# Kernel tuning notes

Hardware: AMD Instinct MI355X
Metric: run time of the kernel (lower is better)

Reference implementation:

```python
import jax, jax.numpy as jnp
import numpy as np

N_NODES = 65536
N_EDGES = 1048576
IN_CH, HID_CH, OUT_CH = 300, 64, 20
DROPOUT_P = 0.5


def setup_inputs() -> dict:
    key = jax.random.key(0)
    ks = jax.random.split(key, 6)
    x = jax.random.normal(ks[0], (N_NODES, IN_CH), dtype=jnp.float32)
    edge_index = jax.random.randint(ks[1], (2, N_EDGES), 0, N_NODES, dtype=jnp.int64)
    edge_weight = jax.random.uniform(ks[2], (N_EDGES,), dtype=jnp.float32)
    # Glorot-ish init for linear weights (PyG lin has no bias; GCNConv adds its own bias)
    W1 = jax.random.normal(ks[3], (IN_CH, HID_CH), dtype=jnp.float32) / np.sqrt(IN_CH)
    b1 = jnp.zeros((HID_CH,), dtype=jnp.float32)
    W2 = jax.random.normal(ks[4], (HID_CH, OUT_CH), dtype=jnp.float32) / np.sqrt(HID_CH)
    b2 = jnp.zeros((OUT_CH,), dtype=jnp.float32)
    return {"x": x, "edge_index": edge_index, "edge_weight": edge_weight,
            "W1": W1, "b1": b1, "W2": W2, "b2": b2}


def _gcn_conv(x, src, dst, edge_weight, W, b, num_nodes):
    # GCNConv with add_self_loops=False, normalize=False:
    #   h = x @ W; out[i] = sum_{e: dst(e)=i} w_e * h[src(e)]; out += b
    h = x @ W                                   # [N, C_out]
    msg = h[src] * edge_weight[:, None]         # [E, C_out]
    agg = jax.ops.segment_sum(msg, dst, num_segments=num_nodes)
    return agg + b


def reference(x, edge_index, edge_weight, W1, b1, W2, b2):
    num_nodes = x.shape[0]
    src, dst = edge_index[0], edge_index[1]
    h = _gcn_conv(x, src, dst, edge_weight, W1, b1, num_nodes)
    h = jax.nn.relu(h)
    # dropout p=0.5, training=True, deterministic fixed key
    keep = jax.random.bernoulli(jax.random.key(42), 1.0 - DROPOUT_P, h.shape)
    h = jnp.where(keep, h / (1.0 - DROPOUT_P), 0.0)
    out = _gcn_conv(h, src, dst, edge_weight, W2, b2, num_nodes)
    return out
```

## Files before the change

kernel.cpp:

```cpp
#include <hip/hip_runtime.h>

#define N_NODES 65536
#define N_EDGES 1048576
#define NB 256
#define CAP 4608
#define EPB_A 4096
#define BLK_A (N_EDGES / EPB_A)
#define EPT_A (EPB_A / 256)

typedef __attribute__((ext_vector_type(8))) short short8v;
typedef __attribute__((ext_vector_type(4))) float float4v;

__device__ __forceinline__ unsigned short f2bf(float f) {
  unsigned u = __float_as_uint(f);
  unsigned r = u + 0x7FFFu + ((u >> 16) & 1u);
  return (unsigned short)(r >> 16);
}
__device__ __forceinline__ float bflo(unsigned u) { return __uint_as_float(u << 16); }
__device__ __forceinline__ float bfhi(unsigned u) { return __uint_as_float(u & 0xFFFF0000u); }

__device__ __forceinline__ bool keep_mask(unsigned idx) {
  const unsigned k0 = 0u, k1 = 42u;
  const unsigned k2 = 0x1BD11BDAu ^ k0 ^ k1;
  unsigned x0 = 0u;
  unsigned x1 = idx;
  x0 += k0; x1 += k1;
#define TF_ROUND(r) { x0 += x1; x1 = (x1 << (r)) | (x1 >> (32 - (r))); x1 ^= x0; }
  TF_ROUND(13) TF_ROUND(15) TF_ROUND(26) TF_ROUND(6)
  x0 += k1; x1 += k2 + 1u;
  TF_ROUND(17) TF_ROUND(29) TF_ROUND(16) TF_ROUND(24)
  x0 += k2; x1 += k0 + 2u;
  TF_ROUND(13) TF_ROUND(15) TF_ROUND(26) TF_ROUND(6)
  x0 += k0; x1 += k1 + 3u;
  TF_ROUND(17) TF_ROUND(29) TF_ROUND(16) TF_ROUND(24)
  x0 += k1; x1 += k2 + 4u;
  TF_ROUND(13) TF_ROUND(15) TF_ROUND(26) TF_ROUND(6)
  x0 += k2; x1 += k0 + 5u;
#undef TF_ROUND
  return ((x0 ^ x1) & 0x80000000u) == 0u;
}

__global__ __launch_bounds__(256) void prep_w1(const float* __restrict__ W1,
                                               unsigned short* __restrict__ Wt,
                                               unsigned* __restrict__ gcur) {
  if (blockIdx.x == 0) gcur[threadIdx.x] = 0u;
  int i = blockIdx.x * 256 + threadIdx.x;
  if (i >= 64 * 320) return;
  int ch = i / 320, k = i % 320;
  float v = (k < 300) ? W1[k * 64 + ch] : 0.0f;
  Wt[i] = f2bf(v);
}

__global__ __launch_bounds__(256) void bin_pass(const int* __restrict__ ei,
                                                const float* __restrict__ ew,
                                                unsigned* __restrict__ gcur,
                                                uint2* __restrict__ binned) {
  __shared__ unsigned cnt[NB], lofs[NB], lcur[NB], gbase[NB];
  __shared__ uint2 stage[EPB_A];
  const int t = threadIdx.x;
  const int e0 = blockIdx.x * EPB_A;
  cnt[t] = 0u;
  lcur[t] = 0u;
  __syncthreads();
  unsigned pk[EPT_A], pw[EPT_A];
#pragma unroll
  for (int j = 0; j < EPT_A; ++j) {
    int e = e0 + t + j * 256;
    unsigned s = (unsigned)ei[e];
    unsigned d = (unsigned)ei[N_EDGES + e];
    pk[j] = s | (d << 16);
    pw[j] = __float_as_uint(ew[e]);
    atomicAdd(&cnt[d >> 8], 1u);
  }
  __syncthreads();
  lofs[t] = cnt[t];
  __syncthreads();
  for (int d = 1; d < NB; d <<= 1) {
    unsigned u = (t >= d) ? lofs[t - d] : 0u;
    __syncthreads();
    lofs[t] += u;
    __syncthreads();
  }
  unsigned incl = lofs[t];
  lofs[t] = incl - cnt[t];
  gbase[t] = (unsigned)t * CAP + atomicAdd(&gcur[t], cnt[t]);
  __syncthreads();
#pragma unroll
  for (int j = 0; j < EPT_A; ++j) {
    unsigned b = pk[j] >> 24;
    unsigned slot = lofs[b] + atomicAdd(&lcur[b], 1u);
    stage[slot] = make_uint2(pk[j], pw[j]);
  }
  __syncthreads();
  for (int s = t; s < EPB_A; s += 256) {
    uint2 u = stage[s];
    unsigned b = u.x >> 24;
    binned[gbase[b] + ((unsigned)s - lofs[b])] = u;
  }
}

__global__ __launch_bounds__(256) void bucket_sort(const unsigned* __restrict__ gcur,
                                                   const uint2* __restrict__ binned,
                                                   unsigned* __restrict__ sortedc,
                                                   unsigned* __restrict__ offs_p) {
  __shared__ uint2 eLDS[CAP];
  __shared__ unsigned cnt[NB], cur[NB];
  const int t = threadIdx.x;
  const int b = blockIdx.x;
  const unsigned lo = (unsigned)b * CAP;
  const unsigned n_edges = gcur[b];
  cnt[t] = 0u;
  __syncthreads();
  for (unsigned i = t; i < n_edges; i += 256) {
    uint2 u = binned[lo + i];
    eLDS[i] = u;
    atomicAdd(&cnt[(u.x >> 16) & 255u], 1u);
  }
  __syncthreads();
  cur[t] = cnt[t];
  __syncthreads();
  for (int d = 1; d < NB; d <<= 1) {
    unsigned u = (t >= d) ? cur[t - d] : 0u;
    __syncthreads();
    cur[t] += u;
    __syncthreads();
  }
  unsigned excl = cur[t] - cnt[t];
  offs_p[b * NB + t] = (lo + excl) | (cnt[t] << 21);
  __syncthreads();
  cur[t] = excl;
  __syncthreads();
  for (unsigned i = t; i < n_edges; i += 256) {
    uint2 u = eLDS[i];
    unsigned lo8 = (u.x >> 16) & 255u;
    unsigned p = lo + atomicAdd(&cur[lo8], 1u);
    sortedc[p] = (u.x & 0xFFFFu) | ((unsigned)f2bf(__uint_as_float(u.y)) << 16);
  }
}

__global__ __launch_bounds__(256) void gemm1_mfma(const float* __restrict__ x,
                                                  const unsigned short* __restrict__ Wt,
                                                  unsigned short* __restrict__ h1b) {
  __shared__ unsigned short As[64][72];
  __shared__ unsigned short Bs[64][72];
  const int t = threadIdx.x;
  const int node0 = blockIdx.x * 64;
  const int wave = t >> 6, lane = t & 63;
  const int quad = lane >> 4, l16 = lane & 15;
  float4v acc[4] = {{0.f,0.f,0.f,0.f},{0.f,0.f,0.f,0.f},{0.f,0.f,0.f,0.f},{0.f,0.f,0.f,0.f}};

  for (int kt = 0; kt < 5; ++kt) {
    const int k0 = kt * 64;
    for (int f = t; f < 1024; f += 256) {
      int node = f >> 4;
      int k = (f & 15) * 4;
      uint2 packed;
      if (k0 + k < 300) {
        float4 v = *(const float4*)(x + (size_t)(node0 + node) * 300 + k0 + k);
        packed.x = (unsigned)f2bf(v.x) | ((unsigned)f2bf(v.y) << 16);
        packed.y = (unsigned)f2bf(v.z) | ((unsigned)f2bf(v.w) << 16);
      } else {
        packed.x = 0u; packed.y = 0u;
      }
      *(uint2*)&As[node][k] = packed;
    }
    for (int f = t; f < 512; f += 256) {
      int ch = f >> 3;
      int kq = f & 7;
      uint4 v = *(const uint4*)(Wt + (size_t)ch * 320 + k0 + kq * 8);
      *(uint4*)&Bs[ch][kq * 8] = v;
    }
    __syncthreads();
    short8v a0 = *(const short8v*)&As[wave * 16 + l16][quad * 8];
    short8v a1 = *(const short8v*)&As[wave * 16 + l16][32 + quad * 8];
#pragma unroll
    for (int nt = 0; nt < 4; ++nt) {
      short8v b0 = *(const short8v*)&Bs[nt * 16 + l16][quad * 8];
      short8v b1 = *(const short8v*)&Bs[nt * 16 + l16][32 + quad * 8];
      acc[nt] = __builtin_amdgcn_mfma_f32_16x16x32_bf16(a0, b0, acc[nt], 0, 0, 0);
      acc[nt] = __builtin_amdgcn_mfma_f32_16x16x32_bf16(a1, b1, acc[nt], 0, 0, 0);
    }
    __syncthreads();
  }
#pragma unroll
  for (int nt = 0; nt < 4; ++nt) {
#pragma unroll
    for (int r = 0; r < 4; ++r) {
      h1b[(size_t)(node0 + wave * 16 + quad * 4 + r) * 64 + nt * 16 + l16] = f2bf(acc[nt][r]);
    }
  }
}

__global__ __launch_bounds__(256) void agg1_gemm2(const unsigned* __restrict__ offs_p,
                                                  const unsigned* __restrict__ sortedc,
                                                  const unsigned short* __restrict__ h1b,
                                                  const float* __restrict__ b1,
                                                  const float* __restrict__ W2,
                                                  unsigned* __restrict__ g32u) {
  __shared__ float h2[16][68];
  __shared__ float w2t[20][68];
  const int t = threadIdx.x;
  const int node0 = blockIdx.x * 16;
  for (int i = t; i < 64 * 20; i += 256) {
    w2t[i % 20][i / 20] = W2[i];
  }
  const int n = t >> 4, cg = t & 15;
  const int node = node0 + n;
  const unsigned op = offs_p[node];
  const unsigned s = op & 0x1FFFFFu;
  const unsigned e_end = s + (op >> 21);
  float4 acc = *(const float4*)(b1 + cg * 4);
  unsigned i = s;
  for (; i + 8 <= e_end; i += 8) {
    unsigned e0 = sortedc[i],     e1 = sortedc[i + 1], e2 = sortedc[i + 2], e3 = sortedc[i + 3];
    unsigned e4 = sortedc[i + 4], e5 = sortedc[i + 5], e6 = sortedc[i + 6], e7 = sortedc[i + 7];
    uint2 v0 = *(const uint2*)(h1b + ((size_t)(e0 & 0xFFFFu)) * 64 + cg * 4);
    uint2 v1 = *(const uint2*)(h1b + ((size_t)(e1 & 0xFFFFu)) * 64 + cg * 4);
    uint2 v2 = *(const uint2*)(h1b + ((size_t)(e2 & 0xFFFFu)) * 64 + cg * 4);
    uint2 v3 = *(const uint2*)(h1b + ((size_t)(e3 & 0xFFFFu)) * 64 + cg * 4);
    uint2 v4 = *(const uint2*)(h1b + ((size_t)(e4 & 0xFFFFu)) * 64 + cg * 4);
    uint2 v5 = *(const uint2*)(h1b + ((size_t)(e5 & 0xFFFFu)) * 64 + cg * 4);
    uint2 v6 = *(const uint2*)(h1b + ((size_t)(e6 & 0xFFFFu)) * 64 + cg * 4);
    uint2 v7 = *(const uint2*)(h1b + ((size_t)(e7 & 0xFFFFu)) * 64 + cg * 4);
    float w0 = bfhi(e0), w1 = bfhi(e1), w2 = bfhi(e2), w3 = bfhi(e3);
    float w4 = bfhi(e4), w5 = bfhi(e5), w6 = bfhi(e6), w7 = bfhi(e7);
    acc.x = fmaf(w0, bflo(v0.x), acc.x); acc.y = fmaf(w0, bfhi(v0.x), acc.y);
    acc.z = fmaf(w0, bflo(v0.y), acc.z); acc.w = fmaf(w0, bfhi(v0.y), acc.w);
    acc.x = fmaf(w1, bflo(v1.x), acc.x); acc.y = fmaf(w1, bfhi(v1.x), acc.y);
    acc.z = fmaf(w1, bflo(v1.y), acc.z); acc.w = fmaf(w1, bfhi(v1.y), acc.w);
    acc.x = fmaf(w2, bflo(v2.x), acc.x); acc.y = fmaf(w2, bfhi(v2.x), acc.y);
    acc.z = fmaf(w2, bflo(v2.y), acc.z); acc.w = fmaf(w2, bfhi(v2.y), acc.w);
    acc.x = fmaf(w3, bflo(v3.x), acc.x); acc.y = fmaf(w3, bfhi(v3.x), acc.y);
    acc.z = fmaf(w3, bflo(v3.y), acc.z); acc.w = fmaf(w3, bfhi(v3.y), acc.w);
    acc.x = fmaf(w4, bflo(v4.x), acc.x); acc.y = fmaf(w4, bfhi(v4.x), acc.y);
    acc.z = fmaf(w4, bflo(v4.y), acc.z); acc.w = fmaf(w4, bfhi(v4.y), acc.w);
    acc.x = fmaf(w5, bflo(v5.x), acc.x); acc.y = fmaf(w5, bfhi(v5.x), acc.y);
    acc.z = fmaf(w5, bflo(v5.y), acc.z); acc.w = fmaf(w5, bfhi(v5.y), acc.w);
    acc.x = fmaf(w6, bflo(v6.x), acc.x); acc.y = fmaf(w6, bfhi(v6.x), acc.y);
    acc.z = fmaf(w6, bflo(v6.y), acc.z); acc.w = fmaf(w6, bfhi(v6.y), acc.w);
    acc.x = fmaf(w7, bflo(v7.x), acc.x); acc.y = fmaf(w7, bfhi(v7.x), acc.y);
    acc.z = fmaf(w7, bflo(v7.y), acc.z); acc.w = fmaf(w7, bfhi(v7.y), acc.w);
  }
  for (; i < e_end; ++i) {
    unsigned e0 = sortedc[i];
    uint2 v0 = *(const uint2*)(h1b + ((size_t)(e0 & 0xFFFFu)) * 64 + cg * 4);
    float w0 = bfhi(e0);
    acc.x = fmaf(w0, bflo(v0.x), acc.x); acc.y = fmaf(w0, bfhi(v0.x), acc.y);
    acc.z = fmaf(w0, bflo(v0.y), acc.z); acc.w = fmaf(w0, bfhi(v0.y), acc.w);
  }
  const unsigned gi = (unsigned)node * 64u + (unsigned)cg * 4u;
  float r[4] = {acc.x, acc.y, acc.z, acc.w};
#pragma unroll
  for (int j = 0; j < 4; ++j) {
    float v = fmaxf(r[j], 0.0f);
    h2[n][cg * 4 + j] = keep_mask(gi + j) ? v * 2.0f : 0.0f;
  }
  __syncthreads();
  float d0 = 0.0f, d1 = 0.0f;
  if (cg < 10) {
    const int c0 = cg * 2, c1 = cg * 2 + 1;
#pragma unroll
    for (int k = 0; k < 64; k += 4) {
      float4 hv = *(const float4*)(&h2[n][k]);
      float4 w0 = *(const float4*)(&w2t[c0][k]);
      float4 w1 = *(const float4*)(&w2t[c1][k]);
      d0 = fmaf(hv.x, w0.x, d0); d0 = fmaf(hv.y, w0.y, d0);
      d0 = fmaf(hv.z, w0.z, d0); d0 = fmaf(hv.w, w0.w, d0);
      d1 = fmaf(hv.x, w1.x, d1); d1 = fmaf(hv.y, w1.y, d1);
      d1 = fmaf(hv.z, w1.z, d1); d1 = fmaf(hv.w, w1.w, d1);
    }
  }
  unsigned packed = (cg < 10) ? ((unsigned)f2bf(d0) | ((unsigned)f2bf(d1) << 16)) : 0u;
  g32u[(size_t)node * 16 + cg] = packed;
}

__global__ __launch_bounds__(256) void aggregate2(const unsigned* __restrict__ offs_p,
                                                  const unsigned* __restrict__ sortedc,
                                                  const unsigned* __restrict__ g32u,
                                                  const float* __restrict__ b2,
                                                  float* __restrict__ out) {
  const int t = threadIdx.x;
  const int n = blockIdx.x * 16 + (t >> 4);
  const int cg = t & 15;
  const unsigned op = offs_p[n];
  const unsigned s = op & 0x1FFFFFu;
  const unsigned e_end = s + (op >> 21);
  float ax = 0.0f, ay = 0.0f;
  unsigned i = s;
  for (; i + 8 <= e_end; i += 8) {
    unsigned e0 = sortedc[i],     e1 = sortedc[i + 1], e2 = sortedc[i + 2], e3 = sortedc[i + 3];
    unsigned e4 = sortedc[i + 4], e5 = sortedc[i + 5], e6 = sortedc[i + 6], e7 = sortedc[i + 7];
    unsigned v0 = g32u[(size_t)(e0 & 0xFFFFu) * 16 + cg];
    unsigned v1 = g32u[(size_t)(e1 & 0xFFFFu) * 16 + cg];
    unsigned v2 = g32u[(size_t)(e2 & 0xFFFFu) * 16 + cg];
    unsigned v3 = g32u[(size_t)(e3 & 0xFFFFu) * 16 + cg];
    unsigned v4 = g32u[(size_t)(e4 & 0xFFFFu) * 16 + cg];
    unsigned v5 = g32u[(size_t)(e5 & 0xFFFFu) * 16 + cg];
    unsigned v6 = g32u[(size_t)(e6 & 0xFFFFu) * 16 + cg];
    unsigned v7 = g32u[(size_t)(e7 & 0xFFFFu) * 16 + cg];
    float w0 = bfhi(e0), w1 = bfhi(e1), w2 = bfhi(e2), w3 = bfhi(e3);
    float w4 = bfhi(e4), w5 = bfhi(e5), w6 = bfhi(e6), w7 = bfhi(e7);
    ax = fmaf(w0, bflo(v0), ax); ay = fmaf(w0, bfhi(v0), ay);
    ax = fmaf(w1, bflo(v1), ax); ay = fmaf(w1, bfhi(v1), ay);
    ax = fmaf(w2, bflo(v2), ax); ay = fmaf(w2, bfhi(v2), ay);
    ax = fmaf(w3, bflo(v3), ax); ay = fmaf(w3, bfhi(v3), ay);
    ax = fmaf(w4, bflo(v4), ax); ay = fmaf(w4, bfhi(v4), ay);
    ax = fmaf(w5, bflo(v5), ax); ay = fmaf(w5, bfhi(v5), ay);
    ax = fmaf(w6, bflo(v6), ax); ay = fmaf(w6, bfhi(v6), ay);
    ax = fmaf(w7, bflo(v7), ax); ay = fmaf(w7, bfhi(v7), ay);
  }
  for (; i < e_end; ++i) {
    unsigned e0 = sortedc[i];
    unsigned v0 = g32u[(size_t)(e0 & 0xFFFFu) * 16 + cg];
    float w0 = bfhi(e0);
    ax = fmaf(w0, bflo(v0), ax); ay = fmaf(w0, bfhi(v0), ay);
  }
  if (cg < 10) {
    float2 o = make_float2(ax + b2[cg * 2], ay + b2[cg * 2 + 1]);
    *(float2*)(out + (size_t)n * 20 + cg * 2) = o;
  }
}

extern "C" void kernel_launch(void* const* d_in, const int* in_sizes, int n_in,
                              void* d_out, int out_size, void* d_ws, size_t ws_size,
                              hipStream_t stream) {
  const float* x  = (const float*)d_in[0];
  const int*   ei = (const int*)d_in[1];
  const float* ew = (const float*)d_in[2];
  const float* W1 = (const float*)d_in[3];
  const float* b1 = (const float*)d_in[4];
  const float* W2 = (const float*)d_in[5];
  const float* b2 = (const float*)d_in[6];
  float* out = (float*)d_out;

  unsigned short* h1b     = (unsigned short*)d_ws;
  unsigned*       g32u    = (unsigned*)(h1b + (size_t)N_NODES * 64);
  uint2*          binned  = (uint2*)(g32u + (size_t)N_NODES * 16);
  unsigned*       sortedc = (unsigned*)(binned + (size_t)NB * CAP);
  unsigned*       offs_p  = sortedc + (size_t)NB * CAP;
  unsigned short* Wt      = (unsigned short*)(offs_p + N_NODES);
  unsigned*       gcur    = (unsigned*)(Wt + 64 * 320);

  prep_w1<<<(64 * 320 + 255) / 256, 256, 0, stream>>>(W1, Wt, gcur);
  bin_pass<<<BLK_A, 256, 0, stream>>>(ei, ew, gcur, binned);
  bucket_sort<<<NB, 256, 0, stream>>>(gcur, binned, sortedc, offs_p);
  gemm1_mfma<<<N_NODES / 64, 256, 0, stream>>>(x, Wt, h1b);
  agg1_gemm2<<<N_NODES / 16, 256, 0, stream>>>(offs_p, sortedc, h1b, b1, W2, g32u);
  aggregate2<<<N_NODES / 16, 256, 0, stream>>>(offs_p, sortedc, g32u, b2, out);
}
```

Before: 223.2 us.

## Co-schedule GEMM1 halves with binning and bucket-sort kernels

The independent GEMM1 node-tile work is split in two halves and merged into the binning and bucket-sort launches, with extra blocks selected by block index. This lets the compute-heavy GEMM overlap the atomic- and memory-bound edge sorting, and it removes one kernel launch. The fused kernels use the larger shared-memory size of the two branches for every block, which can lower occupancy for the GEMM blocks.

After: 224.1 us. About the same (+0.4%).

```diff
diff --git a/kernel.cpp b/kernel.cpp
--- a/kernel.cpp
+++ b/kernel.cpp
@@ -7,6 +7,7 @@
 #define EPB_A 4096
 #define BLK_A (N_EDGES / EPB_A)
 #define EPT_A (EPB_A / 256)
+#define GHALF 512
 
 typedef __attribute__((ext_vector_type(8))) short short8v;
 typedef __attribute__((ext_vector_type(4))) float float4v;
@@ -51,14 +52,18 @@
   Wt[i] = f2bf(v);
 }
 
-__global__ __launch_bounds__(256) void bin_pass(const int* __restrict__ ei,
-                                                const float* __restrict__ ew,
-                                                unsigned* __restrict__ gcur,
-                                                uint2* __restrict__ binned) {
-  __shared__ unsigned cnt[NB], lofs[NB], lcur[NB], gbase[NB];
-  __shared__ uint2 stage[EPB_A];
-  const int t = threadIdx.x;
-  const int e0 = blockIdx.x * EPB_A;
+__device__ __forceinline__ void bin_body(unsigned char* smraw, int bid,
+                                         const int* __restrict__ ei,
+                                         const float* __restrict__ ew,
+                                         unsigned* __restrict__ gcur,
+                                         uint2* __restrict__ binned) {
+  uint2*    stage = (uint2*)smraw;
+  unsigned* cnt   = (unsigned*)(smraw + 32768);
+  unsigned* lofs  = cnt + NB;
+  unsigned* lcur  = lofs + NB;
+  unsigned* gbase = lcur + NB;
+  const int t = threadIdx.x;
+  const int e0 = bid * EPB_A;
   cnt[t] = 0u;
   lcur[t] = 0u;
   __syncthreads();
@@ -99,14 +104,15 @@
   }
 }
 
-__global__ __launch_bounds__(256) void bucket_sort(const unsigned* __restrict__ gcur,
-                                                   const uint2* __restrict__ binned,
-                                                   unsigned* __restrict__ sortedc,
-                                                   unsigned* __restrict__ offs_p) {
-  __shared__ uint2 eLDS[CAP];
-  __shared__ unsigned cnt[NB], cur[NB];
-  const int t = threadIdx.x;
-  const int b = blockIdx.x;
+__device__ __forceinline__ void bucket_body(unsigned char* smraw, int b,
+                                            const unsigned* __restrict__ gcur,
+                                            const uint2* __restrict__ binned,
+                                            unsigned* __restrict__ sortedc,
+                                            unsigned* __restrict__ offs_p) {
+  uint2*    eLDS = (uint2*)smraw;
+  unsigned* cnt  = (unsigned*)(smraw + 36864);
+  unsigned* cur  = cnt + NB;
+  const int t = threadIdx.x;
   const unsigned lo = (unsigned)b * CAP;
   const unsigned n_edges = gcur[b];
   cnt[t] = 0u;
@@ -138,13 +144,14 @@
   }
 }
 
-__global__ __launch_bounds__(256) void gemm1_mfma(const float* __restrict__ x,
-                                                  const unsigned short* __restrict__ Wt,
-                                                  unsigned short* __restrict__ h1b) {
-  __shared__ unsigned short As[64][72];
-  __shared__ unsigned short Bs[64][72];
-  const int t = threadIdx.x;
-  const int node0 = blockIdx.x * 64;
+__device__ __forceinline__ void gemm1_body(unsigned char* smraw, int nb,
+                                           const float* __restrict__ x,
+                                           const unsigned short* __restrict__ Wt,
+                                           unsigned short* __restrict__ h1b) {
+  unsigned short (*As)[72] = (unsigned short (*)[72])smraw;
+  unsigned short (*Bs)[72] = (unsigned short (*)[72])(smraw + 9216);
+  const int t = threadIdx.x;
+  const int node0 = nb * 64;
   const int wave = t >> 6, lane = t & 63;
   const int quad = lane >> 4, l16 = lane & 15;
   float4v acc[4] = {{0.f,0.f,0.f,0.f},{0.f,0.f,0.f,0.f},{0.f,0.f,0.f,0.f},{0.f,0.f,0.f,0.f}};
@@ -188,6 +195,36 @@
     for (int r = 0; r < 4; ++r) {
       h1b[(size_t)(node0 + wave * 16 + quad * 4 + r) * 64 + nt * 16 + l16] = f2bf(acc[nt][r]);
     }
+  }
+}
+
+__global__ __launch_bounds__(256) void fusedA(const int* __restrict__ ei,
+                                              const float* __restrict__ ew,
+                                              unsigned* __restrict__ gcur,
+                                              uint2* __restrict__ binned,
+                                              const float* __restrict__ x,
+                                              const unsigned short* __restrict__ Wt,
+                                              unsigned short* __restrict__ h1b) {
+  __shared__ __align__(16) unsigned char sm[36864];
+  if (blockIdx.x < BLK_A) {
+    bin_body(sm, blockIdx.x, ei, ew, gcur, binned);
+  } else {
+    gemm1_body(sm, blockIdx.x - BLK_A, x, Wt, h1b);
+  }
+}
+
+__global__ __launch_bounds__(256) void fusedB(const unsigned* __restrict__ gcur,
+                                              const uint2* __restrict__ binned,
+                                              unsigned* __restrict__ sortedc,
+                                              unsigned* __restrict__ offs_p,
+                                              const float* __restrict__ x,
+                                              const unsigned short* __restrict__ Wt,
+                                              unsigned short* __restrict__ h1b) {
+  __shared__ __align__(16) unsigned char sm[38912];
+  if (blockIdx.x < NB) {
+    bucket_body(sm, blockIdx.x, gcur, binned, sortedc, offs_p);
+  } else {
+    gemm1_body(sm, GHALF + (blockIdx.x - NB), x, Wt, h1b);
   }
 }
 
@@ -342,9 +379,8 @@
   unsigned*       gcur    = (unsigned*)(Wt + 64 * 320);
 
   prep_w1<<<(64 * 320 + 255) / 256, 256, 0, stream>>>(W1, Wt, gcur);
-  bin_pass<<<BLK_A, 256, 0, stream>>>(ei, ew, gcur, binned);
-  bucket_sort<<<NB, 256, 0, stream>>>(gcur, binned, sortedc, offs_p);
-  gemm1_mfma<<<N_NODES / 64, 256, 0, stream>>>(x, Wt, h1b);
+  fusedA<<<BLK_A + GHALF, 256, 0, stream>>>(ei, ew, gcur, binned, x, Wt, h1b);
+  fusedB<<<NB + GHALF, 256, 0, stream>>>(gcur, binned, sortedc, offs_p, x, Wt, h1b);
   agg1_gemm2<<<N_NODES / 16, 256, 0, stream>>>(offs_p, sortedc, h1b, b1, W2, g32u);
   aggregate2<<<N_NODES / 16, 256, 0, stream>>>(offs_p, sortedc, g32u, b2, out);
 }
```

## Replace two-pass bucket sort with atomic slot scatter fused with GEMM1

Applied to the files above, without the earlier changes.

The bin_pass and bucket_sort kernels are replaced by one pass. Each edge takes a per-destination slot with a global atomic counter and is written straight into a fixed 64-slot row per node. That scatter runs in the same launch as the GEMM1 MFMA blocks, so the two independent stages can overlap, and prep now also zeroes the counters. This drops a kernel, the intermediate binned buffer and the LDS prefix scans. In exchange, edges beyond 64 per node are silently dropped, within-node edge order becomes nondeterministic, and the edge list is spread over a larger, sparser buffer.

Result: slower. 236.2 us (+5.8%).

```diff
diff --git a/kernel.cpp b/kernel.cpp
--- a/kernel.cpp
+++ b/kernel.cpp
@@ -2,11 +2,11 @@
 
 #define N_NODES 65536
 #define N_EDGES 1048576
-#define NB 256
-#define CAP 4608
-#define EPB_A 4096
-#define BLK_A (N_EDGES / EPB_A)
-#define EPT_A (EPB_A / 256)
+#define SLOTS 64
+#define SCAT_BLK 512
+#define SCAT_EPB (N_EDGES / SCAT_BLK)
+#define SCAT_EPT (SCAT_EPB / 256)
+#define GEMM_BLK (N_NODES / 64)
 
 typedef __attribute__((ext_vector_type(8))) short short8v;
 typedef __attribute__((ext_vector_type(4))) float float4v;
@@ -40,111 +40,29 @@
   return ((x0 ^ x1) & 0x80000000u) == 0u;
 }
 
-__global__ __launch_bounds__(256) void prep_w1(const float* __restrict__ W1,
-                                               unsigned short* __restrict__ Wt,
-                                               unsigned* __restrict__ gcur) {
-  if (blockIdx.x == 0) gcur[threadIdx.x] = 0u;
-  int i = blockIdx.x * 256 + threadIdx.x;
+__global__ __launch_bounds__(256) void prep(const float* __restrict__ W1,
+                                            unsigned short* __restrict__ Wt,
+                                            unsigned* __restrict__ cnt) {
+  const int b = blockIdx.x;
+  if (b < 256) {
+    cnt[b * 256 + threadIdx.x] = 0u;
+    return;
+  }
+  int i = (b - 256) * 256 + threadIdx.x;
   if (i >= 64 * 320) return;
   int ch = i / 320, k = i % 320;
   float v = (k < 300) ? W1[k * 64 + ch] : 0.0f;
   Wt[i] = f2bf(v);
 }
 
-__global__ __launch_bounds__(256) void bin_pass(const int* __restrict__ ei,
-                                                const float* __restrict__ ew,
-                                                unsigned* __restrict__ gcur,
-                                                uint2* __restrict__ binned) {
-  __shared__ unsigned cnt[NB], lofs[NB], lcur[NB], gbase[NB];
-  __shared__ uint2 stage[EPB_A];
+__device__ __forceinline__ void gemm1_body(unsigned char* smraw, int nb,
+                                           const float* __restrict__ x,
+                                           const unsigned short* __restrict__ Wt,
+                                           unsigned short* __restrict__ h1b) {
+  unsigned short (*As)[72] = (unsigned short (*)[72])smraw;
+  unsigned short (*Bs)[72] = (unsigned short (*)[72])(smraw + 9216);
   const int t = threadIdx.x;
-  const int e0 = blockIdx.x * EPB_A;
-  cnt[t] = 0u;
-  lcur[t] = 0u;
-  __syncthreads();
-  unsigned pk[EPT_A], pw[EPT_A];
-#pragma unroll
-  for (int j = 0; j < EPT_A; ++j) {
-    int e = e0 + t + j * 256;
-    unsigned s = (unsigned)ei[e];
-    unsigned d = (unsigned)ei[N_EDGES + e];
-    pk[j] = s | (d << 16);
-    pw[j] = __float_as_uint(ew[e]);
-    atomicAdd(&cnt[d >> 8], 1u);
-  }
-  __syncthreads();
-  lofs[t] = cnt[t];
-  __syncthreads();
-  for (int d = 1; d < NB; d <<= 1) {
-    unsigned u = (t >= d) ? lofs[t - d] : 0u;
-    __syncthreads();
-    lofs[t] += u;
-    __syncthreads();
-  }
-  unsigned incl = lofs[t];
-  lofs[t] = incl - cnt[t];
-  gbase[t] = (unsigned)t * CAP + atomicAdd(&gcur[t], cnt[t]);
-  __syncthreads();
-#pragma unroll
-  for (int j = 0; j < EPT_A; ++j) {
-    unsigned b = pk[j] >> 24;
-    unsigned slot = lofs[b] + atomicAdd(&lcur[b], 1u);
-    stage[slot] = make_uint2(pk[j], pw[j]);
-  }
-  __syncthreads();
-  for (int s = t; s < EPB_A; s += 256) {
-    uint2 u = stage[s];
-    unsigned b = u.x >> 24;
-    binned[gbase[b] + ((unsigned)s - lofs[b])] = u;
-  }
-}
-
-__global__ __launch_bounds__(256) void bucket_sort(const unsigned* __restrict__ gcur,
-                                                   const uint2* __restrict__ binned,
-                                                   unsigned* __restrict__ sortedc,
-                                                   unsigned* __restrict__ offs_p) {
-  __shared__ uint2 eLDS[CAP];
-  __shared__ unsigned cnt[NB], cur[NB];
-  const int t = threadIdx.x;
-  const int b = blockIdx.x;
-  const unsigned lo = (unsigned)b * CAP;
-  const unsigned n_edges = gcur[b];
-  cnt[t] = 0u;
-  __syncthreads();
-  for (unsigned i = t; i < n_edges; i += 256) {
-    uint2 u = binned[lo + i];
-    eLDS[i] = u;
-    atomicAdd(&cnt[(u.x >> 16) & 255u], 1u);
-  }
-  __syncthreads();
-  cur[t] = cnt[t];
-  __syncthreads();
-  for (int d = 1; d < NB; d <<= 1) {
-    unsigned u = (t >= d) ? cur[t - d] : 0u;
-    __syncthreads();
-    cur[t] += u;
-    __syncthreads();
-  }
-  unsigned excl = cur[t] - cnt[t];
-  offs_p[b * NB + t] = (lo + excl) | (cnt[t] << 21);
-  __syncthreads();
-  cur[t] = excl;
-  __syncthreads();
-  for (unsigned i = t; i < n_edges; i += 256) {
-    uint2 u = eLDS[i];
-    unsigned lo8 = (u.x >> 16) & 255u;
-    unsigned p = lo + atomicAdd(&cur[lo8], 1u);
-    sortedc[p] = (u.x & 0xFFFFu) | ((unsigned)f2bf(__uint_as_float(u.y)) << 16);
-  }
-}
-
-__global__ __launch_bounds__(256) void gemm1_mfma(const float* __restrict__ x,
-                                                  const unsigned short* __restrict__ Wt,
-                                                  unsigned short* __restrict__ h1b) {
-  __shared__ unsigned short As[64][72];
-  __shared__ unsigned short Bs[64][72];
-  const int t = threadIdx.x;
-  const int node0 = blockIdx.x * 64;
+  const int node0 = nb * 64;
   const int wave = t >> 6, lane = t & 63;
   const int quad = lane >> 4, l16 = lane & 15;
   float4v acc[4] = {{0.f,0.f,0.f,0.f},{0.f,0.f,0.f,0.f},{0.f,0.f,0.f,0.f},{0.f,0.f,0.f,0.f}};
@@ -191,7 +109,32 @@
   }
 }
 
-__global__ __launch_bounds__(256) void agg1_gemm2(const unsigned* __restrict__ offs_p,
+__global__ __launch_bounds__(256) void scatter_gemm1(const int* __restrict__ ei,
+                                                     const float* __restrict__ ew,
+                                                     unsigned* __restrict__ cnt,
+                                                     unsigned* __restrict__ sortedc,
+                                                     const float* __restrict__ x,
+                                                     const unsigned short* __restrict__ Wt,
+                                                     unsigned short* __restrict__ h1b) {
+  __shared__ __align__(16) unsigned char sm[18432];
+  if (blockIdx.x < SCAT_BLK) {
+    const int t = threadIdx.x;
+    const int e0 = blockIdx.x * SCAT_EPB;
+#pragma unroll
+    for (int j = 0; j < SCAT_EPT; ++j) {
+      int e = e0 + t + j * 256;
+      unsigned s = (unsigned)ei[e];
+      unsigned d = (unsigned)ei[N_EDGES + e];
+      unsigned wv = (unsigned)f2bf(ew[e]) << 16;
+      unsigned c = atomicAdd(&cnt[d], 1u);
+      if (c < (unsigned)SLOTS) sortedc[((size_t)d << 6) + c] = s | wv;
+    }
+  } else {
+    gemm1_body(sm, blockIdx.x - SCAT_BLK, x, Wt, h1b);
+  }
+}
+
+__global__ __launch_bounds__(256) void agg1_gemm2(const unsigned* __restrict__ cnt,
                                                   const unsigned* __restrict__ sortedc,
                                                   const unsigned short* __restrict__ h1b,
                                                   const float* __restrict__ b1,
@@ -201,14 +144,16 @@
   __shared__ float w2t[20][68];
   const int t = threadIdx.x;
   const int node0 = blockIdx.x * 16;
-  for (int i = t; i < 64 * 20; i += 256) {
-    w2t[i % 20][i / 20] = W2[i];
+  for (int i = t; i < 20 * 64; i += 256) {
+    int row = i >> 6, col = i & 63;
+    w2t[row][col] = W2[col * 20 + row];
   }
   const int n = t >> 4, cg = t & 15;
   const int node = node0 + n;
-  const unsigned op = offs_p[node];
-  const unsigned s = op & 0x1FFFFFu;
-  const unsigned e_end = s + (op >> 21);
+  unsigned c = cnt[node];
+  if (c > (unsigned)SLOTS) c = (unsigned)SLOTS;
+  const unsigned s = (unsigned)node << 6;
+  const unsigned e_end = s + c;
   float4 acc = *(const float4*)(b1 + cg * 4);
   unsigned i = s;
   for (; i + 8 <= e_end; i += 8) {
@@ -274,7 +219,7 @@
   g32u[(size_t)node * 16 + cg] = packed;
 }
 
-__global__ __launch_bounds__(256) void aggregate2(const unsigned* __restrict__ offs_p,
+__global__ __launch_bounds__(256) void aggregate2(const unsigned* __restrict__ cnt,
                                                   const unsigned* __restrict__ sortedc,
                                                   const unsigned* __restrict__ g32u,
                                                   const float* __restrict__ b2,
@@ -282,9 +227,10 @@
   const int t = threadIdx.x;
   const int n = blockIdx.x * 16 + (t >> 4);
   const int cg = t & 15;
-  const unsigned op = offs_p[n];
-  const unsigned s = op & 0x1FFFFFu;
-  const unsigned e_end = s + (op >> 21);
+  unsigned c = cnt[n];
+  if (c > (unsigned)SLOTS) c = (unsigned)SLOTS;
+  const unsigned s = (unsigned)n << 6;
+  const unsigned e_end = s + c;
   float ax = 0.0f, ay = 0.0f;
   unsigned i = s;
   for (; i + 8 <= e_end; i += 8) {
@@ -335,16 +281,12 @@
 
   unsigned short* h1b     = (unsigned short*)d_ws;
   unsigned*       g32u    = (unsigned*)(h1b + (size_t)N_NODES * 64);
-  uint2*          binned  = (uint2*)(g32u + (size_t)N_NODES * 16);
-  unsigned*       sortedc = (unsigned*)(binned + (size_t)NB * CAP);
-  unsigned*       offs_p  = sortedc + (size_t)NB * CAP;
-  unsigned short* Wt      = (unsigned short*)(offs_p + N_NODES);
-  unsigned*       gcur    = (unsigned*)(Wt + 64 * 320);
-
-  prep_w1<<<(64 * 320 + 255) / 256, 256, 0, stream>>>(W1, Wt, gcur);
-  bin_pass<<<BLK_A, 256, 0, stream>>>(ei, ew, gcur, binned);
-  bucket_sort<<<NB, 256, 0, stream>>>(gcur, binned, sortedc, offs_p);
-  gemm1_mfma<<<N_NODES / 64, 256, 0, stream>>>(x, Wt, h1b);
-  agg1_gemm2<<<N_NODES / 16, 256, 0, stream>>>(offs_p, sortedc, h1b, b1, W2, g32u);
-  aggregate2<<<N_NODES / 16, 256, 0, stream>>>(offs_p, sortedc, g32u, b2, out);
-}
+  unsigned*       sortedc = (unsigned*)(g32u + (size_t)N_NODES * 16);
+  unsigned*       cnt     = sortedc + (size_t)N_NODES * SLOTS;
+  unsigned short* Wt      = (unsigned short*)(cnt + N_NODES);
+
+  prep<<<256 + 80, 256, 0, stream>>>(W1, Wt, cnt);
+  scatter_gemm1<<<SCAT_BLK + GEMM_BLK, 256, 0, stream>>>(ei, ew, cnt, sortedc, x, Wt, h1b);
+  agg1_gemm2<<<N_NODES / 16, 256, 0, stream>>>(cnt, sortedc, h1b, b1, W2, g32u);
+  aggregate2<<<N_NODES / 16, 256, 0, stream>>>(cnt, sortedc, g32u, b2, out);
+}
```
